# Kernel optimization log

Measured on AMD Instinct MI355X. Metric: run time of the kernel, lower is better.

Reference implementation:

```python
import jax, jax.numpy as jnp
import numpy as np

XI_DIM = 4
LENS = jnp.array([0.5, 0.5, 1.0], dtype=jnp.float32)
NOISE_SCALE = jnp.array([0.01, 0.01], dtype=jnp.float32)
PRIOR_SCALE = jnp.array([0.25, 0.5, 0.5, 0.5], dtype=jnp.float32)
LOG2PI = float(np.log(2.0 * np.pi))
_TRIL_R, _TRIL_C = np.tril_indices(XI_DIM, k=-1)  # strict lower triangle (6 entries)


def _mlp(y, W1, b1, W2, b2, W3, b3):
    h = jax.nn.relu(y @ W1 + b1)
    h = jax.nn.relu(h @ W2 + b2)
    return h @ W3 + b3


def _forward_D(xi):
    # robot-arm forward kinematics; xi: [..., 4] -> end point D: [..., 2]
    a1 = xi[..., 1]
    a2 = a1 + xi[..., 2]
    a3 = a2 + xi[..., 3]
    px = LENS[0] * jnp.cos(a1) + LENS[1] * jnp.cos(a2) + LENS[2] * jnp.cos(a3)
    py = xi[..., 0] + LENS[0] * jnp.sin(a1) + LENS[1] * jnp.sin(a2) + LENS[2] * jnp.sin(a3)
    return jnp.stack([px, py], axis=-1)


def setup_inputs() -> dict:
    key = jax.random.key(0)
    N, P = 524288, 8
    ks = jax.random.split(key, 24)
    # observed data exactly as observed_data(): xi ~ Normal(0, prior_scale), y = f(xi)['D'] + noise
    xi_data = jax.random.normal(ks[0], (N, XI_DIM), dtype=jnp.float32) * PRIOR_SCALE
    y = _forward_D(xi_data) + NOISE_SCALE * jax.random.normal(ks[1], (N, 2), dtype=jnp.float32)
    zs = jax.random.normal(ks[2], (N, P, XI_DIM), dtype=jnp.float32)
    inp = {"y": y, "zs": zs}
    base = [("W1", (2, 20)), ("b1", (20,)), ("W2", (20, 10)), ("b2", (10,))]
    i = 3
    for pre, out_dim in (("mu", XI_DIM), ("ld", XI_DIM), ("lo", XI_DIM * (XI_DIM + 1) // 2 - XI_DIM)):
        for nm, sh in base + [("W3", (10, out_dim)), ("b3", (out_dim,))]:
            inp[f"{pre}_{nm}"] = jax.random.normal(ks[i], sh, dtype=jnp.float32) * 0.3
            i += 1
    return inp


def reference(y, zs,
              mu_W1, mu_b1, mu_W2, mu_b2, mu_W3, mu_b3,
              ld_W1, ld_b1, ld_W2, ld_b2, ld_W3, ld_b3,
              lo_W1, lo_b1, lo_W2, lo_b2, lo_W3, lo_b3):
    N, P, D = zs.shape
    q_mu = _mlp(y, mu_W1, mu_b1, mu_W2, mu_b2, mu_W3, mu_b3)                  # [N, 4]
    q_L_diag = jax.nn.softplus(_mlp(y, ld_W1, ld_b1, ld_W2, ld_b2, ld_W3, ld_b3))  # [N, 4]
    q_L_off = _mlp(y, lo_W1, lo_b1, lo_W2, lo_b2, lo_W3, lo_b3)               # [N, 6]
    # batched Cholesky factors L: [N, 4, 4]
    L = jnp.zeros((N, D, D), dtype=y.dtype)
    L = L.at[:, _TRIL_R, _TRIL_C].set(q_L_off)
    di = jnp.arange(D)
    L = L.at[:, di, di].set(q_L_diag)
    # reparameterized samples: xi = mu + L @ z, vectorized over (N, P)
    xi = q_mu[:, None, :] + jnp.einsum('nij,npj->npi', L, zs)                 # [N, P, 4]
    # prior log-prob (independent Normal(0, prior_scale)), summed over dims
    log_prior = jnp.sum(-0.5 * (xi / PRIOR_SCALE) ** 2 - jnp.log(PRIOR_SCALE) - 0.5 * LOG2PI, axis=-1)
    # likelihood: Normal(f(xi)['D'], noise_scale).log_prob(y), summed over y_dim
    Dpt = _forward_D(xi)                                                      # [N, P, 2]
    r = (y[:, None, :] - Dpt) / NOISE_SCALE
    log_lik = jnp.sum(-0.5 * r ** 2 - jnp.log(NOISE_SCALE) - 0.5 * LOG2PI, axis=-1)
    datafit = jnp.mean(log_prior + log_lik, axis=1)                           # [N]
    # MVN entropy with scale_tril L: 0.5*d*(1+log 2pi) + sum log diag(L)
    entropy = 0.5 * D * (1.0 + LOG2PI) + jnp.sum(jnp.log(q_L_diag), axis=-1)
    return jnp.mean(datafit + entropy)
```

## Files before the change

### kernel.cpp

```cpp
#include <hip/hip_runtime.h>
#include <math.h>

#define C_ALL 12.838199208f

struct WPtrs { const float* p[18]; };

__device__ __forceinline__ float softplus_f(float x) {
    return fmaxf(x, 0.0f) + __logf(1.0f + __expf(-fabsf(x)));
}

template <int OD>
__device__ __forceinline__ void mlp1(const float* __restrict__ W1,
                                     const float* __restrict__ b1,
                                     const float* __restrict__ W2,
                                     const float* __restrict__ b2,
                                     const float* __restrict__ W3,
                                     const float* __restrict__ b3,
                                     float y0, float y1, float* out) {
    float h2[10];
#pragma unroll
    for (int k = 0; k < 10; ++k) h2[k] = b2[k];
#pragma unroll
    for (int j = 0; j < 20; ++j) {
        const float h1 = fmaxf(0.0f, fmaf(y0, W1[j], fmaf(y1, W1[20 + j], b1[j])));
#pragma unroll
        for (int k = 0; k < 10; ++k) h2[k] = fmaf(h1, W2[j * 10 + k], h2[k]);
    }
#pragma unroll
    for (int k = 0; k < 10; ++k) h2[k] = fmaxf(0.0f, h2[k]);
#pragma unroll
    for (int d = 0; d < OD; ++d) out[d] = b3[d];
#pragma unroll
    for (int k = 0; k < 10; ++k) {
#pragma unroll
        for (int d = 0; d < OD; ++d) out[d] = fmaf(h2[k], W3[k * OD + d], out[d]);
    }
}

__global__ __launch_bounds__(256) void avi_kernel(
    const float* __restrict__ y, const float* __restrict__ zs, WPtrs wp,
    float* __restrict__ out, int N, float invN) {
    __shared__ float wsum[4];

    const int tid = threadIdx.x;
    const int n = blockIdx.x * 256 + tid;
    float rv = 0.0f;
    if (n < N) {
        const float2 yv = *reinterpret_cast<const float2*>(y + 2 * (size_t)n);
        const float y0 = yv.x, y1 = yv.y;

        const float4* zp = reinterpret_cast<const float4*>(zs + (size_t)n * 32);
        float4 z[8];
#pragma unroll
        for (int p = 0; p < 8; ++p) z[p] = zp[p];
        __builtin_amdgcn_sched_barrier(0);

        float mu[4], ld[4], lo[6];
        mlp1<4>(wp.p[0], wp.p[1], wp.p[2], wp.p[3], wp.p[4], wp.p[5], y0, y1, mu);
        mlp1<4>(wp.p[6], wp.p[7], wp.p[8], wp.p[9], wp.p[10], wp.p[11], y0, y1, ld);
        mlp1<6>(wp.p[12], wp.p[13], wp.p[14], wp.p[15], wp.p[16], wp.p[17], y0, y1, lo);

        const float d0 = softplus_f(ld[0]);
        const float d1 = softplus_f(ld[1]);
        const float d2 = softplus_f(ld[2]);
        const float d3 = softplus_f(ld[3]);
        const float sumlogdiag = __logf(d0 * d1 * d2 * d3);
        const float L10 = lo[0], L20 = lo[1], L21 = lo[2];
        const float L30 = lo[3], L31 = lo[4], L32 = lo[5];

        float acc = 0.0f;
#pragma unroll
        for (int p = 0; p < 8; ++p) {
            const float xi0 = fmaf(d0, z[p].x, mu[0]);
            const float xi1 = fmaf(d1, z[p].y, fmaf(L10, z[p].x, mu[1]));
            const float xi2 = fmaf(d2, z[p].z, fmaf(L21, z[p].y, fmaf(L20, z[p].x, mu[2])));
            const float xi3 = fmaf(d3, z[p].w, fmaf(L32, z[p].z, fmaf(L31, z[p].y, fmaf(L30, z[p].x, mu[3]))));

            const float a1 = xi1, a2 = xi1 + xi2, a3 = a2 + xi3;
            float s1, c1, s2, c2, s3, c3;
            __sincosf(a1, &s1, &c1);
            __sincosf(a2, &s2, &c2);
            __sincosf(a3, &s3, &c3);
            const float px = fmaf(0.5f, c1, fmaf(0.5f, c2, c3));
            const float py = xi0 + fmaf(0.5f, s1, fmaf(0.5f, s2, s3));

            const float q0 = xi0 * 4.0f, q1 = xi1 * 2.0f, q2 = xi2 * 2.0f, q3 = xi3 * 2.0f;
            const float pq = fmaf(q0, q0, fmaf(q1, q1, fmaf(q2, q2, q3 * q3)));
            const float r0 = (y0 - px) * 100.0f;
            const float r1 = (y1 - py) * 100.0f;
            acc = fmaf(-0.5f, pq + fmaf(r0, r0, r1 * r1), acc);
        }
        rv = fmaf(0.125f, acc, C_ALL + sumlogdiag);
    }

#pragma unroll
    for (int d = 32; d > 0; d >>= 1) rv += __shfl_down(rv, d);
    if ((tid & 63) == 0) wsum[tid >> 6] = rv;
    __syncthreads();
    if (tid == 0) {
        const float s = wsum[0] + wsum[1] + wsum[2] + wsum[3];
        atomicAdd(out, s * invN);
    }
}

extern "C" void kernel_launch(void* const* d_in, const int* in_sizes, int n_in,
                              void* d_out, int out_size, void* d_ws, size_t ws_size,
                              hipStream_t stream) {
    const float* y = (const float*)d_in[0];
    const float* zs = (const float*)d_in[1];
    WPtrs wp;
    for (int i = 0; i < 18; ++i) wp.p[i] = (const float*)d_in[2 + i];
    float* out = (float*)d_out;
    const int N = in_sizes[0] / 2;

    hipMemsetAsync(out, 0, sizeof(float), stream);
    const int blocks = (N + 255) / 256;
    avi_kernel<<<blocks, 256, 0, stream>>>(y, zs, wp, out, N, 1.0f / (float)N);
}
```

Measured before the change: 161.6 us.

## Split MLP into packed-FMA params kernel and separate sampling tail kernel

Moves the three per-row MLPs into a separate kernel that handles four rows per thread, using two-wide float vectors so the compiler can emit packed FP32 FMAs, and writes 16 floats of parameters per row to workspace. A second kernel reads these parameters together with zs and does the sampling and likelihood reduction. The aim is to roughly halve MLP instruction count through packed math, but it adds a workspace write and read of 64 bytes per row and an extra kernel launch.

```diff
diff --git a/kernel.cpp b/kernel.cpp
--- a/kernel.cpp
+++ b/kernel.cpp
@@ -3,19 +3,63 @@
 
 #define C_ALL 12.838199208f
 
+typedef float v2 __attribute__((ext_vector_type(2)));
+static __device__ __forceinline__ v2 splat(float s) { return (v2){s, s}; }
+#define FMA2 __builtin_elementwise_fma
+#define MAX2 __builtin_elementwise_max
+
 struct WPtrs { const float* p[18]; };
 
 __device__ __forceinline__ float softplus_f(float x) {
     return fmaxf(x, 0.0f) + __logf(1.0f + __expf(-fabsf(x)));
 }
+__device__ __forceinline__ v2 sp2(v2 x) {
+    v2 r; r.x = softplus_f(x.x); r.y = softplus_f(x.y); return r;
+}
 
 template <int OD>
-__device__ __forceinline__ void mlp1(const float* __restrict__ W1,
+__device__ __forceinline__ void mlp4(const float* __restrict__ W1,
                                      const float* __restrict__ b1,
                                      const float* __restrict__ W2,
                                      const float* __restrict__ b2,
                                      const float* __restrict__ W3,
                                      const float* __restrict__ b3,
+                                     v2 Y0a, v2 Y1a, v2 Y0b, v2 Y1b,
+                                     v2* oa, v2* ob) {
+    v2 h2a[10], h2b[10];
+#pragma unroll
+    for (int k = 0; k < 10; ++k) { const v2 bb = splat(b2[k]); h2a[k] = bb; h2b[k] = bb; }
+#pragma unroll
+    for (int j = 0; j < 20; ++j) {
+        const float w0 = W1[j], w1 = W1[20 + j], bb = b1[j];
+        const v2 h1a = MAX2(FMA2(Y0a, splat(w0), FMA2(Y1a, splat(w1), splat(bb))), splat(0.0f));
+        const v2 h1b = MAX2(FMA2(Y0b, splat(w0), FMA2(Y1b, splat(w1), splat(bb))), splat(0.0f));
+#pragma unroll
+        for (int k = 0; k < 10; ++k) {
+            const v2 w = splat(W2[j * 10 + k]);
+            h2a[k] = FMA2(h1a, w, h2a[k]);
+            h2b[k] = FMA2(h1b, w, h2b[k]);
+        }
+    }
+#pragma unroll
+    for (int k = 0; k < 10; ++k) { h2a[k] = MAX2(h2a[k], splat(0.0f)); h2b[k] = MAX2(h2b[k], splat(0.0f)); }
+#pragma unroll
+    for (int d = 0; d < OD; ++d) { const v2 bb = splat(b3[d]); oa[d] = bb; ob[d] = bb; }
+#pragma unroll
+    for (int k = 0; k < 10; ++k) {
+#pragma unroll
+        for (int d = 0; d < OD; ++d) {
+            const v2 w = splat(W3[k * OD + d]);
+            oa[d] = FMA2(h2a[k], w, oa[d]);
+            ob[d] = FMA2(h2b[k], w, ob[d]);
+        }
+    }
+}
+
+template <int OD>
+__device__ __forceinline__ void mlp1(const float* __restrict__ W1, const float* __restrict__ b1,
+                                     const float* __restrict__ W2, const float* __restrict__ b2,
+                                     const float* __restrict__ W3, const float* __restrict__ b3,
                                      float y0, float y1, float* out) {
     float h2[10];
 #pragma unroll
@@ -31,21 +75,85 @@
 #pragma unroll
     for (int d = 0; d < OD; ++d) out[d] = b3[d];
 #pragma unroll
-    for (int k = 0; k < 10; ++k) {
+    for (int k = 0; k < 10; ++k)
 #pragma unroll
         for (int d = 0; d < OD; ++d) out[d] = fmaf(h2[k], W3[k * OD + d], out[d]);
-    }
-}
-
-__global__ __launch_bounds__(256) void avi_kernel(
-    const float* __restrict__ y, const float* __restrict__ zs, WPtrs wp,
-    float* __restrict__ out, int N, float invN) {
+}
+
+__device__ __forceinline__ void store_params(float* __restrict__ pr, int row,
+                                             float m0, float m1, float m2, float m3,
+                                             float d0, float d1, float d2, float d3,
+                                             float L10, float L20, float L21,
+                                             float L30, float L31, float L32) {
+    float4* q = reinterpret_cast<float4*>(pr + (size_t)row * 16);
+    q[0] = make_float4(m0, m1, m2, m3);
+    q[1] = make_float4(d0, d1, d2, d3);
+    q[2] = make_float4(L10, L20, L21, L30);
+    q[3] = make_float4(L31, L32, __logf(d0 * d1 * d2 * d3), 0.0f);
+}
+
+__global__ __launch_bounds__(256) void avi_params(
+    const float* __restrict__ y, WPtrs wp, float* __restrict__ pr, int N) {
+    const int tid = threadIdx.x;
+    const int r0 = blockIdx.x * 1024 + tid;
+
+    if (r0 + 768 < N) {
+        const float2 ya = *reinterpret_cast<const float2*>(y + 2 * (size_t)(r0));
+        const float2 yb = *reinterpret_cast<const float2*>(y + 2 * (size_t)(r0 + 256));
+        const float2 yc = *reinterpret_cast<const float2*>(y + 2 * (size_t)(r0 + 512));
+        const float2 yd = *reinterpret_cast<const float2*>(y + 2 * (size_t)(r0 + 768));
+        const v2 Y0a = {ya.x, yb.x}, Y1a = {ya.y, yb.y};
+        const v2 Y0b = {yc.x, yd.x}, Y1b = {yc.y, yd.y};
+
+        v2 mua[4], mub[4], lda[4], ldb[4], loa[6], lob[6];
+        mlp4<4>(wp.p[0], wp.p[1], wp.p[2], wp.p[3], wp.p[4], wp.p[5],
+                Y0a, Y1a, Y0b, Y1b, mua, mub);
+        mlp4<4>(wp.p[6], wp.p[7], wp.p[8], wp.p[9], wp.p[10], wp.p[11],
+                Y0a, Y1a, Y0b, Y1b, lda, ldb);
+        mlp4<6>(wp.p[12], wp.p[13], wp.p[14], wp.p[15], wp.p[16], wp.p[17],
+                Y0a, Y1a, Y0b, Y1b, loa, lob);
+
+        const v2 da0 = sp2(lda[0]), da1 = sp2(lda[1]), da2 = sp2(lda[2]), da3 = sp2(lda[3]);
+        const v2 db0 = sp2(ldb[0]), db1 = sp2(ldb[1]), db2 = sp2(ldb[2]), db3 = sp2(ldb[3]);
+
+        store_params(pr, r0,       mua[0].x, mua[1].x, mua[2].x, mua[3].x,
+                     da0.x, da1.x, da2.x, da3.x,
+                     loa[0].x, loa[1].x, loa[2].x, loa[3].x, loa[4].x, loa[5].x);
+        store_params(pr, r0 + 256, mua[0].y, mua[1].y, mua[2].y, mua[3].y,
+                     da0.y, da1.y, da2.y, da3.y,
+                     loa[0].y, loa[1].y, loa[2].y, loa[3].y, loa[4].y, loa[5].y);
+        store_params(pr, r0 + 512, mub[0].x, mub[1].x, mub[2].x, mub[3].x,
+                     db0.x, db1.x, db2.x, db3.x,
+                     lob[0].x, lob[1].x, lob[2].x, lob[3].x, lob[4].x, lob[5].x);
+        store_params(pr, r0 + 768, mub[0].y, mub[1].y, mub[2].y, mub[3].y,
+                     db0.y, db1.y, db2.y, db3.y,
+                     lob[0].y, lob[1].y, lob[2].y, lob[3].y, lob[4].y, lob[5].y);
+    } else {
+        for (int s = 0; s < 4; ++s) {
+            const int row = r0 + s * 256;
+            if (row >= N) continue;
+            const float2 yv = *reinterpret_cast<const float2*>(y + 2 * (size_t)row);
+            float mu[4], ld[4], lo[6];
+            mlp1<4>(wp.p[0], wp.p[1], wp.p[2], wp.p[3], wp.p[4], wp.p[5], yv.x, yv.y, mu);
+            mlp1<4>(wp.p[6], wp.p[7], wp.p[8], wp.p[9], wp.p[10], wp.p[11], yv.x, yv.y, ld);
+            mlp1<6>(wp.p[12], wp.p[13], wp.p[14], wp.p[15], wp.p[16], wp.p[17], yv.x, yv.y, lo);
+            store_params(pr, row, mu[0], mu[1], mu[2], mu[3],
+                         softplus_f(ld[0]), softplus_f(ld[1]), softplus_f(ld[2]), softplus_f(ld[3]),
+                         lo[0], lo[1], lo[2], lo[3], lo[4], lo[5]);
+        }
+    }
+}
+
+__global__ __launch_bounds__(256) void avi_tail(
+    const float* __restrict__ y, const float* __restrict__ zs,
+    const float* __restrict__ pr, float* __restrict__ out, int N, float invN) {
     __shared__ float wsum[4];
-
     const int tid = threadIdx.x;
     const int n = blockIdx.x * 256 + tid;
     float rv = 0.0f;
     if (n < N) {
+        const float4* pq = reinterpret_cast<const float4*>(pr + (size_t)n * 16);
+        const float4 p0 = pq[0], p1 = pq[1], p2 = pq[2], p3 = pq[3];
         const float2 yv = *reinterpret_cast<const float2*>(y + 2 * (size_t)n);
         const float y0 = yv.x, y1 = yv.y;
 
@@ -55,26 +163,18 @@
         for (int p = 0; p < 8; ++p) z[p] = zp[p];
         __builtin_amdgcn_sched_barrier(0);
 
-        float mu[4], ld[4], lo[6];
-        mlp1<4>(wp.p[0], wp.p[1], wp.p[2], wp.p[3], wp.p[4], wp.p[5], y0, y1, mu);
-        mlp1<4>(wp.p[6], wp.p[7], wp.p[8], wp.p[9], wp.p[10], wp.p[11], y0, y1, ld);
-        mlp1<6>(wp.p[12], wp.p[13], wp.p[14], wp.p[15], wp.p[16], wp.p[17], y0, y1, lo);
-
-        const float d0 = softplus_f(ld[0]);
-        const float d1 = softplus_f(ld[1]);
-        const float d2 = softplus_f(ld[2]);
-        const float d3 = softplus_f(ld[3]);
-        const float sumlogdiag = __logf(d0 * d1 * d2 * d3);
-        const float L10 = lo[0], L20 = lo[1], L21 = lo[2];
-        const float L30 = lo[3], L31 = lo[4], L32 = lo[5];
+        const float m0 = p0.x, m1 = p0.y, m2 = p0.z, m3 = p0.w;
+        const float d0 = p1.x, d1 = p1.y, d2 = p1.z, d3 = p1.w;
+        const float L10 = p2.x, L20 = p2.y, L21 = p2.z, L30 = p2.w;
+        const float L31 = p3.x, L32 = p3.y, slog = p3.z;
 
         float acc = 0.0f;
 #pragma unroll
         for (int p = 0; p < 8; ++p) {
-            const float xi0 = fmaf(d0, z[p].x, mu[0]);
-            const float xi1 = fmaf(d1, z[p].y, fmaf(L10, z[p].x, mu[1]));
-            const float xi2 = fmaf(d2, z[p].z, fmaf(L21, z[p].y, fmaf(L20, z[p].x, mu[2])));
-            const float xi3 = fmaf(d3, z[p].w, fmaf(L32, z[p].z, fmaf(L31, z[p].y, fmaf(L30, z[p].x, mu[3]))));
+            const float xi0 = fmaf(d0, z[p].x, m0);
+            const float xi1 = fmaf(d1, z[p].y, fmaf(L10, z[p].x, m1));
+            const float xi2 = fmaf(d2, z[p].z, fmaf(L21, z[p].y, fmaf(L20, z[p].x, m2)));
+            const float xi3 = fmaf(d3, z[p].w, fmaf(L32, z[p].z, fmaf(L31, z[p].y, fmaf(L30, z[p].x, m3))));
 
             const float a1 = xi1, a2 = xi1 + xi2, a3 = a2 + xi3;
             float s1, c1, s2, c2, s3, c3;
@@ -85,12 +185,12 @@
             const float py = xi0 + fmaf(0.5f, s1, fmaf(0.5f, s2, s3));
 
             const float q0 = xi0 * 4.0f, q1 = xi1 * 2.0f, q2 = xi2 * 2.0f, q3 = xi3 * 2.0f;
-            const float pq = fmaf(q0, q0, fmaf(q1, q1, fmaf(q2, q2, q3 * q3)));
+            const float pq2 = fmaf(q0, q0, fmaf(q1, q1, fmaf(q2, q2, q3 * q3)));
             const float r0 = (y0 - px) * 100.0f;
             const float r1 = (y1 - py) * 100.0f;
-            acc = fmaf(-0.5f, pq + fmaf(r0, r0, r1 * r1), acc);
-        }
-        rv = fmaf(0.125f, acc, C_ALL + sumlogdiag);
+            acc = fmaf(-0.5f, pq2 + fmaf(r0, r0, r1 * r1), acc);
+        }
+        rv = fmaf(0.125f, acc, C_ALL + slog);
     }
 
 #pragma unroll
@@ -111,9 +211,10 @@
     WPtrs wp;
     for (int i = 0; i < 18; ++i) wp.p[i] = (const float*)d_in[2 + i];
     float* out = (float*)d_out;
+    float* pr = (float*)d_ws;
     const int N = in_sizes[0] / 2;
 
     hipMemsetAsync(out, 0, sizeof(float), stream);
-    const int blocks = (N + 255) / 256;
-    avi_kernel<<<blocks, 256, 0, stream>>>(y, zs, wp, out, N, 1.0f / (float)N);
-}
+    avi_params<<<(N + 1023) / 1024, 256, 0, stream>>>(y, wp, pr, N);
+    avi_tail<<<(N + 255) / 256, 256, 0, stream>>>(y, zs, pr, out, N, 1.0f / (float)N);
+}
```

Measured after the change: 183.5 us. 13.6% more time.
